# Performance work log

Hardware: AMD Instinct MI355X
Metric: run time of the kernel (lower is better)

Reference implementation:

```python
import jax, jax.numpy as jnp
import numpy as np

B, P, H = 256, 100, 512
NH, HD = 16, 32          # n_head, head_dim
V, N = 20, 200
VN = 1 + V + N           # 221
CSD = 16                 # cur_status_dim
SCALE = HD ** (-0.5)


def setup_inputs() -> dict:
    key = jax.random.key(0)
    ks = jax.random.split(key, 16)
    inp = {
        "q_global": jax.random.normal(ks[0], (B, P, H), jnp.float32),
        "k_global": jax.random.normal(ks[1], (B, NH, VN, HD), jnp.float32),
        "v_global": jax.random.normal(ks[2], (B, NH, VN, HD), jnp.float32),
        "k_node": jax.random.normal(ks[3], (B, NH, 1 + N, HD), jnp.float32),
        "v_node": jax.random.normal(ks[4], (B, NH, 1 + N, HD), jnp.float32),
        "k_vehicle": jax.random.normal(ks[5], (B, NH, 1 + V, HD), jnp.float32),
        "v_vehicle": jax.random.normal(ks[6], (B, NH, 1 + V, HD), jnp.float32),
        "k_vehicle_node": jax.random.normal(ks[7], (B, NH, V, HD), jnp.float32),
        "v_vehicle_node": jax.random.normal(ks[8], (B, NH, V, HD), jnp.float32),
        "context_feature": jax.random.normal(ks[9], (B, P, CSD), jnp.float32),
        "cache_pointer": jax.random.normal(ks[10], (B, H, VN), jnp.float32),
    }
    # random illegal mask; keep the depot column (0) always legal so no row is fully masked
    mask = jax.random.bernoulli(ks[11], 0.3, (B * P, VN))
    inp["illegal_mask"] = mask.at[:, 0].set(False)
    # learned params (torch Linear stores [out, in])
    inp["Wq_w"] = jax.random.normal(ks[12], (H, H + CSD), jnp.float32) * 0.02
    inp["combine_w"] = jax.random.normal(ks[13], (H, H), jnp.float32) * 0.02
    inp["combine_b"] = jax.random.normal(ks[14], (H,), jnp.float32) * 0.02
    return inp


def _attend(q, k, v, mask=None):
    # q: [B,NH,P,HD], k/v: [B,NH,K,HD], mask: [B,P,K] bool (True = illegal)
    scores = jnp.einsum("bhpd,bhkd->bhpk", q, k) * SCALE
    if mask is not None:
        scores = jnp.where(mask[:, None, :, :], -jnp.inf, scores)
    w = jax.nn.softmax(scores, axis=-1)
    ctx = jnp.einsum("bhpk,bhkd->bhpd", w, v)
    return ctx.transpose(0, 2, 1, 3).reshape(q.shape[0], q.shape[2], NH * HD)  # [B,P,H]


def reference(q_global, k_global, v_global, k_node, v_node, k_vehicle, v_vehicle,
              k_vehicle_node, v_vehicle_node, context_feature, cache_pointer,
              illegal_mask, Wq_w, combine_w, combine_b):
    mask = illegal_mask.reshape(B, P, VN)
    q = jnp.concatenate([q_global, context_feature], axis=-1) @ Wq_w.T  # [B,P,H]
    q = q.reshape(B, P, NH, HD).transpose(0, 2, 1, 3)                   # [B,NH,P,HD]
    context = (_attend(q, k_global, v_global, mask)
               + _attend(q, k_node, v_node)
               + _attend(q, k_vehicle, v_vehicle)
               + _attend(q, k_vehicle_node, v_vehicle_node))            # [B,P,H]
    mha_out = context @ combine_w.T + combine_b                          # [B,P,H]
    logits = jnp.einsum("bph,bhk->bpk", mha_out, cache_pointer)          # [B,P,VN]
    return logits.reshape(B * P, VN).astype(jnp.float32)
```

## Files before the change

kernel.cpp:

```cpp
#include <hip/hip_runtime.h>
#include <hip/hip_bf16.h>

#define B_   256
#define P_   100
#define H_   512
#define NH_  16
#define HD_  32
#define VN_  221
#define KNODE 201
#define KVEH  21
#define KVND  20
#define CSD_ 16
#define MASKP 224

typedef __attribute__((ext_vector_type(8))) short short8;
typedef __attribute__((ext_vector_type(4))) float f32x4;

#define K_OFF   0
#define V_OFF   38400
#define ATTN_LDS_B 69632

__device__ __forceinline__ unsigned cvtpk(float lo, float hi) {
    unsigned r;
    asm("v_cvt_pk_bf16_f32 %0, %1, %2" : "=v"(r) : "v"(lo), "v"(hi));
    return r;
}
__device__ __forceinline__ unsigned f2bf(float f) {
    union { float f; unsigned u; } x; x.f = f;
    return (x.u + 0x7FFFu + ((x.u >> 16) & 1u)) >> 16;
}

__global__ void mask_detect_kernel(const unsigned int* __restrict__ w,
                                   int nwords, int* __restrict__ flag) {
    int i = blockIdx.x * 256 + threadIdx.x;
    if (i < nwords && (w[i] & ~1u)) atomicOr(flag, 1);
}

__global__ void mask_repack_kernel(const unsigned char* __restrict__ mb,
                                   const int* __restrict__ mw,
                                   const int* __restrict__ flag,
                                   unsigned char* __restrict__ out) {
    int i = blockIdx.x * blockDim.x + threadIdx.x;
    if (i >= B_ * P_ * MASKP) return;
    int row = i / MASKP, k = i - row * MASKP;
    unsigned char v = 1;
    if (k < VN_) {
        int src = row * VN_ + k;
        v = (*flag) ? (unsigned char)(mb[src] != 0) : (unsigned char)(mw[src] != 0);
    }
    out[i] = v;
}

template<bool MASKED, int C0, int C1, int LO, int HI>
__device__ __forceinline__ void attend_v5(
    const char* __restrict__ ldsb,
    const unsigned* __restrict__ mpre,
    short8 qf, int g, int qr, int addrA, int addrB,
    f32x4& O0, f32x4& O1)
{
    f32x4 A0a = {0.f,0.f,0.f,0.f}, A1a = {0.f,0.f,0.f,0.f};
    f32x4 A0b = {0.f,0.f,0.f,0.f}, A1b = {0.f,0.f,0.f,0.f};
    float ssum = 0.f;
    const bool sel = g < 2;
    #pragma unroll
    for (int c = C0; c <= C1; ++c) {
        const int kb = c * 32;
        short8 kf0 = *(const short8*)(ldsb + K_OFF + (size_t)(kb + qr) * 80 + g * 16);
        short8 kf1 = *(const short8*)(ldsb + K_OFF + (size_t)(kb + 16 + qr) * 80 + g * 16);
        __builtin_amdgcn_s_setprio(1);
        f32x4 s0 = __builtin_amdgcn_mfma_f32_16x16x32_bf16(
                       kf0, qf, (f32x4){0.f,0.f,0.f,0.f}, 0, 0, 0);
        f32x4 s1 = __builtin_amdgcn_mfma_f32_16x16x32_bf16(
                       kf1, qf, (f32x4){0.f,0.f,0.f,0.f}, 0, 0, 0);
        __builtin_amdgcn_s_setprio(0);
        unsigned mdw0 = 0, mdw1 = 0;
        if (MASKED) {
            mdw0 = mpre[2 * (c - C0)];
            mdw1 = mpre[2 * (c - C0) + 1];
        }
        float e0[4], e1[4];
        #pragma unroll
        for (int r = 0; r < 4; ++r) {
            const int key0 = kb + 4 * g + r;
            const int key1 = key0 + 16;
            float x0 = exp2f(s0[r]);
            float x1 = exp2f(s1[r]);
            bool ok0, ok1;
            if (MASKED) {
                ok0 = ((mdw0 >> (8 * r)) & 255u) == 0u;
                ok1 = ((mdw1 >> (8 * r)) & 255u) == 0u;
            } else {
                ok0 = (key0 >= LO) & (key0 < HI);
                ok1 = (key1 >= LO) & (key1 < HI);
            }
            e0[r] = ok0 ? x0 : 0.f;
            e1[r] = ok1 ? x1 : 0.f;
            ssum += e0[r] + e1[r];
        }
        unsigned w0 = cvtpk(e0[0], e0[1]), w1 = cvtpk(e0[2], e0[3]);
        unsigned w2 = cvtpk(e1[0], e1[1]), w3 = cvtpk(e1[2], e1[3]);
        int pA0 = __builtin_amdgcn_ds_bpermute(addrA, (int)w0);
        int pA1 = __builtin_amdgcn_ds_bpermute(addrA, (int)w1);
        int pB0 = __builtin_amdgcn_ds_bpermute(addrB, (int)w0);
        int pB1 = __builtin_amdgcn_ds_bpermute(addrB, (int)w1);
        int qA0 = __builtin_amdgcn_ds_bpermute(addrA, (int)w2);
        int qA1 = __builtin_amdgcn_ds_bpermute(addrA, (int)w3);
        int qB0 = __builtin_amdgcn_ds_bpermute(addrB, (int)w2);
        int qB1 = __builtin_amdgcn_ds_bpermute(addrB, (int)w3);
        union { int u[4]; short8 s8; } pf;
        pf.u[0] = sel ? pA0 : qA0;
        pf.u[1] = sel ? pA1 : qA1;
        pf.u[2] = sel ? pB0 : qB0;
        pf.u[3] = sel ? pB1 : qB1;
        short8 v0 = *(const short8*)(ldsb + V_OFF + (size_t)qr * 976 + kb * 2 + g * 16);
        short8 v1 = *(const short8*)(ldsb + V_OFF + (size_t)(qr + 16) * 976 + kb * 2 + g * 16);
        __builtin_amdgcn_s_setprio(1);
        if (c & 1) {
            A0b = __builtin_amdgcn_mfma_f32_16x16x32_bf16(v0, pf.s8, A0b, 0, 0, 0);
            A1b = __builtin_amdgcn_mfma_f32_16x16x32_bf16(v1, pf.s8, A1b, 0, 0, 0);
        } else {
            A0a = __builtin_amdgcn_mfma_f32_16x16x32_bf16(v0, pf.s8, A0a, 0, 0, 0);
            A1a = __builtin_amdgcn_mfma_f32_16x16x32_bf16(v1, pf.s8, A1a, 0, 0, 0);
        }
        __builtin_amdgcn_s_setprio(0);
    }
    ssum += __shfl_xor(ssum, 16);
    ssum += __shfl_xor(ssum, 32);
    const float inv = 1.f / ssum;
    O0 += (A0a + A0b) * inv;
    O1 += (A1a + A1b) * inv;
}

__global__ __launch_bounds__(512, 4) void attn_mfma_kernel(
    const float* __restrict__ q4,
    const float* __restrict__ kg,  const float* __restrict__ vg,
    const float* __restrict__ kn,  const float* __restrict__ vn,
    const float* __restrict__ kv,  const float* __restrict__ vv,
    const float* __restrict__ kvn, const float* __restrict__ vvn,
    const unsigned char* __restrict__ maskp,
    float* __restrict__ ctx_out)
{
    extern __shared__ char ldsb[];
    const int tid = threadIdx.x;
    const int bh = blockIdx.x, b = bh >> 4, nh = bh & 15;

    const int wave = tid >> 6;
    const int g = (tid >> 4) & 3, qr = tid & 15;
    const int q0 = wave * 16;
    const int qe = (q0 + qr < 100) ? (q0 + qr) : 99;
    const float* qp = q4 + ((size_t)bh * 100 + qe) * 32 + g * 8;
    float4 qa = *(const float4*)qp;
    float4 qc = *(const float4*)(qp + 4);
    const unsigned char* mrow = maskp + ((size_t)b * 100 + qe) * MASKP;
    unsigned mpre[14];
    #pragma unroll
    for (int c = 0; c < 7; ++c) {
        mpre[2 * c]     = *(const unsigned*)(mrow + c * 32 + g * 4);
        mpre[2 * c + 1] = *(const unsigned*)(mrow + c * 32 + 16 + g * 4);
    }

    const float* kg_s  = kg  + (size_t)bh * VN_   * 32;
    const float* kn_s  = kn  + (size_t)bh * KNODE * 32;
    const float* kv_s  = kv  + (size_t)bh * KVEH  * 32;
    const float* kvn_s = kvn + (size_t)bh * KVND  * 32;
    const float* vg_s  = vg  + (size_t)bh * VN_   * 32;
    const float* vn_s  = vn  + (size_t)bh * KNODE * 32;
    const float* vv_s  = vv  + (size_t)bh * KVEH  * 32;
    const float* vvn_s = vvn + (size_t)bh * KVND  * 32;

    {
        float4 ka[4], kc[4];
        int koff[4]; bool kok[4];
        #pragma unroll
        for (int it = 0; it < 4; ++it) {
            int slot = tid + it * 512;
            kok[it] = slot < 1852;
            const float* sp; int li, r0;
            if (slot >= 1772)      { sp = kvn_s; li = slot - 1772; r0 = 456; }
            else if (slot >= 1688) { sp = kv_s;  li = slot - 1688; r0 = 432; }
            else if (slot >= 884)  { sp = kn_s;  li = slot - 884;  r0 = 224; }
            else                   { sp = kg_s;  li = slot;        r0 = 0;   }
            int r = li >> 2, s2 = li & 3;
            koff[it] = (r0 + r) * 80 + s2 * 16;
            if (kok[it]) {
                ka[it] = *(const float4*)(sp + r * 32 + s2 * 8);
                kc[it] = *(const float4*)(sp + r * 32 + s2 * 8 + 4);
            }
        }
        #pragma unroll
        for (int it = 0; it < 4; ++it) {
            if (kok[it]) {
                uint4 w;
                w.x = cvtpk(ka[it].x, ka[it].y); w.y = cvtpk(ka[it].z, ka[it].w);
                w.z = cvtpk(kc[it].x, kc[it].y); w.w = cvtpk(kc[it].z, kc[it].w);
                *(uint4*)(ldsb + K_OFF + koff[it]) = w;
            }
        }
    }
    for (int lin = tid; lin < 17 * 4; lin += 512) {
        int zi = lin >> 2, s = lin & 3;
        int zr = (zi < 3) ? 221 + zi : (zi < 10) ? 422 + zi
               : (zi < 13) ? 443 + zi : 463 + zi;
        *(uint4*)(ldsb + K_OFF + (size_t)zr * 80 + s * 16) = (uint4){0,0,0,0};
    }
    {
        char* vb = ldsb + V_OFF;
        float4 va[4], vb4[4];
        int vd0[4], vk2[4]; bool vok[4];
        #pragma unroll
        for (int it = 0; it < 4; ++it) {
            int slot = tid + it * 512;
            vok[it] = slot < 1840;
            const float* sp; int li, r0;
            if (slot >= 1760)      { sp = vvn_s; li = slot - 1760; r0 = 456; }
            else if (slot >= 1680) { sp = vv_s;  li = slot - 1680; r0 = 432; }
            else if (slot >= 880)  { sp = vn_s;  li = slot - 880;  r0 = 224; }
            else                   { sp = vg_s;  li = slot;        r0 = 0;   }
            int p = li >> 3, dq = li & 7;
            vd0[it] = dq * 4;
            vk2[it] = (r0 + 2 * p) * 2;
            if (vok[it]) {
                va[it]  = *(const float4*)(sp + (2 * p) * 32 + dq * 4);
                vb4[it] = *(const float4*)(sp + (2 * p + 1) * 32 + dq * 4);
            }
        }
        #pragma unroll
        for (int it = 0; it < 4; ++it) {
            if (vok[it]) {
                int d0 = vd0[it], k2 = vk2[it];
                *(unsigned*)(vb + (size_t)(d0 + 0) * 976 + k2) = cvtpk(va[it].x, vb4[it].x);
                *(unsigned*)(vb + (size_t)(d0 + 1) * 976 + k2) = cvtpk(va[it].y, vb4[it].y);
                *(unsigned*)(vb + (size_t)(d0 + 2) * 976 + k2) = cvtpk(va[it].z, vb4[it].z);
                *(unsigned*)(vb + (size_t)(d0 + 3) * 976 + k2) = cvtpk(va[it].w, vb4[it].w);
            }
        }
        if (tid < 32) {
            int d = tid;
            *(unsigned*)(vb + (size_t)d * 976 + 220 * 2) = cvtpk(vg_s[220 * 32 + d], 0.f);
            *(unsigned*)(vb + (size_t)d * 976 + 424 * 2) = cvtpk(vn_s[200 * 32 + d], 0.f);
            *(unsigned*)(vb + (size_t)d * 976 + 452 * 2) = cvtpk(vv_s[20 * 32 + d], 0.f);
        }
        for (int lin = tid; lin < 7 * 32; lin += 512) {
            int pi = lin >> 5, d = lin & 31;
            int pk = (pi == 0) ? 222 : (pi < 4) ? 424 + 2 * pi
                   : (pi == 4) ? 454 : 466 + 2 * pi;
            *(unsigned*)(vb + (size_t)d * 976 + (size_t)pk * 2) = 0;
        }
    }
    __syncthreads();

    if (wave >= 7) return;

    short8 qf;
    {
        const float SC = 0.2550524218f;
        union { unsigned u[4]; short8 s8; } q;
        q.u[0] = cvtpk(qa.x * SC, qa.y * SC);
        q.u[1] = cvtpk(qa.z * SC, qa.w * SC);
        q.u[2] = cvtpk(qc.x * SC, qc.y * SC);
        q.u[3] = cvtpk(qc.z * SC, qc.w * SC);
        qf = q.s8;
    }
    const int addrA = 4 * (qr + ((g & 1) << 5));
    const int addrB = addrA + 64;

    f32x4 O0 = {0.f,0.f,0.f,0.f}, O1 = {0.f,0.f,0.f,0.f};
    attend_v5<true,  0,  6,   0, 224>(ldsb, mpre, qf, g, qr, addrA, addrB, O0, O1);
    attend_v5<false, 7, 13, 224, 425>(ldsb, nullptr, qf, g, qr, addrA, addrB, O0, O1);
    attend_v5<false,13, 14, 432, 453>(ldsb, nullptr, qf, g, qr, addrA, addrB, O0, O1);
    attend_v5<false,14, 14, 456, 476>(ldsb, nullptr, qf, g, qr, addrA, addrB, O0, O1);

    if (q0 + qr < 100) {
        float* op = ctx_out + ((size_t)b * 100 + q0 + qr) * 512 + nh * 32 + 4 * g;
        *(f32x4*)op        = O0;
        *(f32x4*)(op + 16) = O1;
    }
}

template<bool QPROJ>
__global__ __launch_bounds__(512, 4) void gemm_nfused(
    const float* __restrict__ Aq, const float* __restrict__ cf,
    const float* __restrict__ W,  const float* __restrict__ bias,
    float* __restrict__ outp)
{
    __shared__ char As[64 * 80];
    __shared__ char Bs[256 * 80];
    const int tid = threadIdx.x;
    const int n0 = blockIdx.x * 256, m0 = blockIdx.y * 64;
    const int wave = tid >> 6, lane = tid & 63;
    const int wm = wave >> 2, wn = wave & 3;
    const int g = lane >> 4, qr = lane & 15;
    const int ar = tid >> 3, as = tid & 7;
    constexpr int KTOT_ = QPROJ ? 544 : 512;
    constexpr int WSTR  = QPROJ ? 528 : 512;

    f32x4 acc[2][4] = {};
    for (int k0 = 0; k0 < KTOT_; k0 += 32) {
        float4 a4 = {0,0,0,0};
        {
            const int k = k0 + as * 4;
            if (!QPROJ || k < 512) {
                a4 = *(const float4*)(Aq + (size_t)(m0 + ar) * 512 + k);
            } else if (k < 528) {
                a4 = *(const float4*)(cf + (size_t)(m0 + ar) * 16 + (k - 512));
            }
        }
        float4 b0[2], b1[2];
        #pragma unroll
        for (int it = 0; it < 2; ++it) {
            int slot = tid + it * 512;
            int row = slot >> 2, sq = slot & 3;
            int k = k0 + sq * 8;
            b0[it] = (float4){0,0,0,0}; b1[it] = (float4){0,0,0,0};
            if (!QPROJ || k < 528) {
                const float* wp = W + (size_t)(n0 + row) * WSTR + k;
                b0[it] = *(const float4*)wp;
                b1[it] = *(const float4*)(wp + 4);
            }
        }
        __syncthreads();
        {
            uint2 w;
            w.x = cvtpk(a4.x, a4.y); w.y = cvtpk(a4.z, a4.w);
            *(uint2*)(As + ar * 80 + as * 8) = w;
        }
        #pragma unroll
        for (int it = 0; it < 2; ++it) {
            int slot = tid + it * 512;
            int row = slot >> 2, sq = slot & 3;
            uint4 w;
            w.x = cvtpk(b0[it].x, b0[it].y); w.y = cvtpk(b0[it].z, b0[it].w);
            w.z = cvtpk(b1[it].x, b1[it].y); w.w = cvtpk(b1[it].z, b1[it].w);
            *(uint4*)(Bs + row * 80 + sq * 16) = w;
        }
        __syncthreads();
        short8 af0 = *(const short8*)(As + (wm * 32 + qr) * 80 + g * 16);
        short8 af1 = *(const short8*)(As + (wm * 32 + 16 + qr) * 80 + g * 16);
        #pragma unroll
        for (int nj = 0; nj < 4; ++nj) {
            short8 bf = *(const short8*)(Bs + (wn * 64 + nj * 16 + qr) * 80 + g * 16);
            acc[0][nj] = __builtin_amdgcn_mfma_f32_16x16x32_bf16(af0, bf, acc[0][nj], 0, 0, 0);
            acc[1][nj] = __builtin_amdgcn_mfma_f32_16x16x32_bf16(af1, bf, acc[1][nj], 0, 0, 0);
        }
    }
    #pragma unroll
    for (int mi = 0; mi < 2; ++mi)
        #pragma unroll
        for (int nj = 0; nj < 4; ++nj) {
            const int n = n0 + wn * 64 + nj * 16 + qr;
            const float bia = QPROJ ? 0.f : bias[n];
            #pragma unroll
            for (int reg = 0; reg < 4; ++reg) {
                int m = m0 + wm * 32 + 16 * mi + 4 * g + reg;
                if (QPROJ) {
                    int bb = m / 100, p = m - bb * 100;
                    int nh = n >> 5, d = n & 31;
                    outp[(((size_t)bb * NH_ + nh) * P_ + p) * HD_ + d] = acc[mi][nj][reg];
                } else {
                    outp[(size_t)m * 512 + n] = acc[mi][nj][reg] + bia;
                }
            }
        }
}

__global__ __launch_bounds__(512, 4) void logits_mfma(
    const float* __restrict__ mha,
    const float* __restrict__ cp,
    float* __restrict__ out)
{
    __shared__ char As[128 * 80];
    __shared__ char Bs[112 * 80];
    const int b   = blockIdx.x >> 1;
    const int nh0 = (blockIdx.x & 1) * 112;
    const int tid = threadIdx.x;
    const int wave = tid >> 6, lane = tid & 63;
    const int g = lane >> 4, qr = lane & 15;
    const int row = tid >> 2, s = tid & 3;

    f32x4 acc[7] = {};
    for (int h0 = 0; h0 < 512; h0 += 32) {
        float4 a4 = {0,0,0,0}, c4 = {0,0,0,0};
        if (row < 100) {
            const float* mp = mha + ((size_t)b * P_ + row) * 512 + h0 + 8 * s;
            a4 = *(const float4*)mp;
            c4 = *(const float4*)(mp + 4);
        }
        float cv[2][4];
        int ckk[2], chq[2]; bool cok[2];
        #pragma unroll
        for (int it = 0; it < 2; ++it) {
            int slot = tid + it * 512;
            bool in = slot < 896;
            int kkl = in ? (slot % 112) : 0;
            int hq  = in ? (slot / 112) : 0;
            int kk  = nh0 + kkl;
            ckk[it] = kkl; chq[it] = hq;
            cok[it] = in;
            cv[it][0] = cv[it][1] = cv[it][2] = cv[it][3] = 0.f;
            if (in && kk < VN_) {
                const float* cpp = cp + ((size_t)b * 512 + h0 + hq * 4) * VN_ + kk;
                cv[it][0] = cpp[0];
                cv[it][1] = cpp[VN_];
                cv[it][2] = cpp[2 * VN_];
                cv[it][3] = cpp[3 * VN_];
            }
        }
        __syncthreads();
        {
            uint4 w;
            w.x = cvtpk(a4.x, a4.y); w.y = cvtpk(a4.z, a4.w);
            w.z = cvtpk(c4.x, c4.y); w.w = cvtpk(c4.z, c4.w);
            *(uint4*)(As + row * 80 + s * 16) = w;
        }
        #pragma unroll
        for (int it = 0; it < 2; ++it) {
            if (cok[it]) {
                uint2 w;
                w.x = cvtpk(cv[it][0], cv[it][1]);
                w.y = cvtpk(cv[it][2], cv[it][3]);
                *(uint2*)(Bs + ckk[it] * 80 + chq[it] * 8) = w;
            }
        }
        __syncthreads();
        short8 af = *(const short8*)(As + (wave * 16 + qr) * 80 + g * 16);
        #pragma unroll
        for (int ni = 0; ni < 7; ++ni) {
            short8 bf = *(const short8*)(Bs + (ni * 16 + qr) * 80 + g * 16);
            acc[ni] = __builtin_amdgcn_mfma_f32_16x16x32_bf16(af, bf, acc[ni], 0, 0, 0);
        }
    }
    #pragma unroll
    for (int ni = 0; ni < 7; ++ni) {
        int key = nh0 + ni * 16 + qr;
        if (key >= VN_) continue;
        #pragma unroll
        for (int reg = 0; reg < 4; ++reg) {
            int p = wave * 16 + 4 * g + reg;
            if (p < P_)
                out[((size_t)b * P_ + p) * VN_ + key] = acc[ni][reg];
        }
    }
}

extern "C" void kernel_launch(void* const* d_in, const int* in_sizes, int n_in,
                              void* d_out, int out_size, void* d_ws, size_t ws_size,
                              hipStream_t stream) {
    const float* qg   = (const float*)d_in[0];
    const float* kgl  = (const float*)d_in[1];
    const float* vgl  = (const float*)d_in[2];
    const float* knd  = (const float*)d_in[3];
    const float* vnd  = (const float*)d_in[4];
    const float* kvh  = (const float*)d_in[5];
    const float* vvh  = (const float*)d_in[6];
    const float* kvnd = (const float*)d_in[7];
    const float* vvnd = (const float*)d_in[8];
    const float* cf   = (const float*)d_in[9];
    const float* cp   = (const float*)d_in[10];
    const void*  mask_raw = d_in[11];
    const float* Wq   = (const float*)d_in[12];
    const float* Wc   = (const float*)d_in[13];
    const float* bias = (const float*)d_in[14];
    float* out = (float*)d_out;

    const size_t NQ = (size_t)B_ * NH_ * P_ * HD_;
    float* q4buf  = (float*)d_ws;
    float* ctxbuf = q4buf + NQ;
    float* mhabuf = q4buf;
    unsigned char* mask8 = (unsigned char*)(ctxbuf + NQ);
    const int MASKN_P = B_ * P_ * MASKP;
    int* flag = (int*)(mask8 + ((MASKN_P + 15) & ~15));

    hipFuncSetAttribute(reinterpret_cast<const void*>(attn_mfma_kernel),
                        hipFuncAttributeMaxDynamicSharedMemorySize,
                        ATTN_LDS_B);

    hipMemsetAsync(flag, 0, sizeof(int), stream);
    mask_detect_kernel<<<16, 256, 0, stream>>>(
        (const unsigned int*)mask_raw, 4096, flag);
    mask_repack_kernel<<<(MASKN_P + 255) / 256, 256, 0, stream>>>(
        (const unsigned char*)mask_raw, (const int*)mask_raw, flag, mask8);

    gemm_nfused<true><<<dim3(2, 400), 512, 0, stream>>>(qg, cf, Wq, nullptr, q4buf);
    attn_mfma_kernel<<<B_ * NH_, 512, ATTN_LDS_B, stream>>>(
        q4buf, kgl, vgl, knd, vnd, kvh, vvh, kvnd, vvnd, mask8, ctxbuf);
    gemm_nfused<false><<<dim3(2, 400), 512, 0, stream>>>(ctxbuf, nullptr, Wc, bias, mhabuf);
    logits_mfma<<<B_ * 2, 512, 0, stream>>>(mhabuf, cp, out);
}
```

Measured before the change: 337.6 us.

## Make attention kernel persistent with double-buffered LDS prefetch of next head

Replaces the one-block-per-(batch,head) attention launch with 256 persistent blocks, each looping over 16 heads. Each block keeps two LDS buffers and loads the next head's K/V (converted to bf16) and Q while it computes the current one, hiding global load latency behind MFMA work. The mask is now read per chunk instead of prefetched into registers. The cost is twice the LDS per block, which lowers occupancy to one block per CU, and only 256 blocks on a device with more CUs may leave some idle.

New measurement: 691.3 us. 105% more time.

```diff
diff --git a/kernel.cpp b/kernel.cpp
--- a/kernel.cpp
+++ b/kernel.cpp
@@ -19,6 +19,7 @@
 #define K_OFF   0
 #define V_OFF   38400
 #define ATTN_LDS_B 69632
+#define ATTN_LDS_2B (2 * ATTN_LDS_B)
 
 __device__ __forceinline__ unsigned cvtpk(float lo, float hi) {
     unsigned r;
@@ -51,10 +52,108 @@
     out[i] = v;
 }
 
+__device__ __forceinline__ void k_issue(
+    float4 (&ka)[4], float4 (&kc)[4], int (&koff)[4], bool (&kok)[4],
+    int tid, int bh,
+    const float* __restrict__ kg, const float* __restrict__ kn,
+    const float* __restrict__ kv, const float* __restrict__ kvn)
+{
+    const float* kg_s  = kg  + (size_t)bh * VN_   * 32;
+    const float* kn_s  = kn  + (size_t)bh * KNODE * 32;
+    const float* kv_s  = kv  + (size_t)bh * KVEH  * 32;
+    const float* kvn_s = kvn + (size_t)bh * KVND  * 32;
+    #pragma unroll
+    for (int it = 0; it < 4; ++it) {
+        int slot = tid + it * 512;
+        kok[it] = slot < 1852;
+        const float* sp; int li, r0;
+        if (slot >= 1772)      { sp = kvn_s; li = slot - 1772; r0 = 456; }
+        else if (slot >= 1688) { sp = kv_s;  li = slot - 1688; r0 = 432; }
+        else if (slot >= 884)  { sp = kn_s;  li = slot - 884;  r0 = 224; }
+        else                   { sp = kg_s;  li = slot;        r0 = 0;   }
+        int r = li >> 2, s2 = li & 3;
+        koff[it] = (r0 + r) * 80 + s2 * 16;
+        if (kok[it]) {
+            ka[it] = *(const float4*)(sp + r * 32 + s2 * 8);
+            kc[it] = *(const float4*)(sp + r * 32 + s2 * 8 + 4);
+        }
+    }
+}
+__device__ __forceinline__ void k_write(
+    const float4 (&ka)[4], const float4 (&kc)[4],
+    const int (&koff)[4], const bool (&kok)[4], char* __restrict__ ldsb)
+{
+    #pragma unroll
+    for (int it = 0; it < 4; ++it) {
+        if (kok[it]) {
+            uint4 w;
+            w.x = cvtpk(ka[it].x, ka[it].y); w.y = cvtpk(ka[it].z, ka[it].w);
+            w.z = cvtpk(kc[it].x, kc[it].y); w.w = cvtpk(kc[it].z, kc[it].w);
+            *(uint4*)(ldsb + K_OFF + koff[it]) = w;
+        }
+    }
+}
+__device__ __forceinline__ void v_issue(
+    float4 (&va)[4], float4 (&vc)[4], int (&vd0)[4], int (&vk2)[4], bool (&vok)[4],
+    float (&tl)[3],
+    int tid, int bh,
+    const float* __restrict__ vg, const float* __restrict__ vn,
+    const float* __restrict__ vv, const float* __restrict__ vvn)
+{
+    const float* vg_s  = vg  + (size_t)bh * VN_   * 32;
+    const float* vn_s  = vn  + (size_t)bh * KNODE * 32;
+    const float* vv_s  = vv  + (size_t)bh * KVEH  * 32;
+    const float* vvn_s = vvn + (size_t)bh * KVND  * 32;
+    #pragma unroll
+    for (int it = 0; it < 4; ++it) {
+        int slot = tid + it * 512;
+        vok[it] = slot < 1840;
+        const float* sp; int li, r0;
+        if (slot >= 1760)      { sp = vvn_s; li = slot - 1760; r0 = 456; }
+        else if (slot >= 1680) { sp = vv_s;  li = slot - 1680; r0 = 432; }
+        else if (slot >= 880)  { sp = vn_s;  li = slot - 880;  r0 = 224; }
+        else                   { sp = vg_s;  li = slot;        r0 = 0;   }
+        int p = li >> 3, dq = li & 7;
+        vd0[it] = dq * 4;
+        vk2[it] = (r0 + 2 * p) * 2;
+        if (vok[it]) {
+            va[it] = *(const float4*)(sp + (2 * p) * 32 + dq * 4);
+            vc[it] = *(const float4*)(sp + (2 * p + 1) * 32 + dq * 4);
+        }
+    }
+    if (tid < 32) {
+        tl[0] = vg_s[220 * 32 + tid];
+        tl[1] = vn_s[200 * 32 + tid];
+        tl[2] = vv_s[20 * 32 + tid];
+    }
+}
+__device__ __forceinline__ void v_write(
+    const float4 (&va)[4], const float4 (&vc)[4],
+    const int (&vd0)[4], const int (&vk2)[4], const bool (&vok)[4],
+    const float (&tl)[3], char* __restrict__ ldsb, int tid)
+{
+    char* vb = ldsb + V_OFF;
+    #pragma unroll
+    for (int it = 0; it < 4; ++it) {
+        if (vok[it]) {
+            int d0 = vd0[it], k2 = vk2[it];
+            *(unsigned*)(vb + (size_t)(d0 + 0) * 976 + k2) = cvtpk(va[it].x, vc[it].x);
+            *(unsigned*)(vb + (size_t)(d0 + 1) * 976 + k2) = cvtpk(va[it].y, vc[it].y);
+            *(unsigned*)(vb + (size_t)(d0 + 2) * 976 + k2) = cvtpk(va[it].z, vc[it].z);
+            *(unsigned*)(vb + (size_t)(d0 + 3) * 976 + k2) = cvtpk(va[it].w, vc[it].w);
+        }
+    }
+    if (tid < 32) {
+        *(unsigned*)(vb + (size_t)tid * 976 + 220 * 2) = cvtpk(tl[0], 0.f);
+        *(unsigned*)(vb + (size_t)tid * 976 + 424 * 2) = cvtpk(tl[1], 0.f);
+        *(unsigned*)(vb + (size_t)tid * 976 + 452 * 2) = cvtpk(tl[2], 0.f);
+    }
+}
+
 template<bool MASKED, int C0, int C1, int LO, int HI>
-__device__ __forceinline__ void attend_v5(
+__device__ __forceinline__ void attend_v6(
     const char* __restrict__ ldsb,
-    const unsigned* __restrict__ mpre,
+    const unsigned char* __restrict__ mrow,
     short8 qf, int g, int qr, int addrA, int addrB,
     f32x4& O0, f32x4& O1)
 {
@@ -75,8 +174,8 @@
         __builtin_amdgcn_s_setprio(0);
         unsigned mdw0 = 0, mdw1 = 0;
         if (MASKED) {
-            mdw0 = mpre[2 * (c - C0)];
-            mdw1 = mpre[2 * (c - C0) + 1];
+            mdw0 = *(const unsigned*)(mrow + kb + g * 4);
+            mdw1 = *(const unsigned*)(mrow + kb + 16 + g * 4);
         }
         float e0[4], e1[4];
         #pragma unroll
@@ -131,7 +230,7 @@
     O1 += (A1a + A1b) * inv;
 }
 
-__global__ __launch_bounds__(512, 4) void attn_mfma_kernel(
+__global__ __launch_bounds__(512, 4) void attn_persist(
     const float* __restrict__ q4,
     const float* __restrict__ kg,  const float* __restrict__ vg,
     const float* __restrict__ kn,  const float* __restrict__ vn,
@@ -140,106 +239,24 @@
     const unsigned char* __restrict__ maskp,
     float* __restrict__ ctx_out)
 {
-    extern __shared__ char ldsb[];
+    extern __shared__ char lds2[];
     const int tid = threadIdx.x;
-    const int bh = blockIdx.x, b = bh >> 4, nh = bh & 15;
-
-    const int wave = tid >> 6;
-    const int g = (tid >> 4) & 3, qr = tid & 15;
+    const int wave = tid >> 6, g = (tid >> 4) & 3, qr = tid & 15;
     const int q0 = wave * 16;
     const int qe = (q0 + qr < 100) ? (q0 + qr) : 99;
-    const float* qp = q4 + ((size_t)bh * 100 + qe) * 32 + g * 8;
-    float4 qa = *(const float4*)qp;
-    float4 qc = *(const float4*)(qp + 4);
-    const unsigned char* mrow = maskp + ((size_t)b * 100 + qe) * MASKP;
-    unsigned mpre[14];
-    #pragma unroll
-    for (int c = 0; c < 7; ++c) {
-        mpre[2 * c]     = *(const unsigned*)(mrow + c * 32 + g * 4);
-        mpre[2 * c + 1] = *(const unsigned*)(mrow + c * 32 + 16 + g * 4);
-    }
-
-    const float* kg_s  = kg  + (size_t)bh * VN_   * 32;
-    const float* kn_s  = kn  + (size_t)bh * KNODE * 32;
-    const float* kv_s  = kv  + (size_t)bh * KVEH  * 32;
-    const float* kvn_s = kvn + (size_t)bh * KVND  * 32;
-    const float* vg_s  = vg  + (size_t)bh * VN_   * 32;
-    const float* vn_s  = vn  + (size_t)bh * KNODE * 32;
-    const float* vv_s  = vv  + (size_t)bh * KVEH  * 32;
-    const float* vvn_s = vvn + (size_t)bh * KVND  * 32;
-
-    {
-        float4 ka[4], kc[4];
-        int koff[4]; bool kok[4];
-        #pragma unroll
-        for (int it = 0; it < 4; ++it) {
-            int slot = tid + it * 512;
-            kok[it] = slot < 1852;
-            const float* sp; int li, r0;
-            if (slot >= 1772)      { sp = kvn_s; li = slot - 1772; r0 = 456; }
-            else if (slot >= 1688) { sp = kv_s;  li = slot - 1688; r0 = 432; }
-            else if (slot >= 884)  { sp = kn_s;  li = slot - 884;  r0 = 224; }
-            else                   { sp = kg_s;  li = slot;        r0 = 0;   }
-            int r = li >> 2, s2 = li & 3;
-            koff[it] = (r0 + r) * 80 + s2 * 16;
-            if (kok[it]) {
-                ka[it] = *(const float4*)(sp + r * 32 + s2 * 8);
-                kc[it] = *(const float4*)(sp + r * 32 + s2 * 8 + 4);
-            }
-        }
-        #pragma unroll
-        for (int it = 0; it < 4; ++it) {
-            if (kok[it]) {
-                uint4 w;
-                w.x = cvtpk(ka[it].x, ka[it].y); w.y = cvtpk(ka[it].z, ka[it].w);
-                w.z = cvtpk(kc[it].x, kc[it].y); w.w = cvtpk(kc[it].z, kc[it].w);
-                *(uint4*)(ldsb + K_OFF + koff[it]) = w;
-            }
-        }
-    }
-    for (int lin = tid; lin < 17 * 4; lin += 512) {
-        int zi = lin >> 2, s = lin & 3;
-        int zr = (zi < 3) ? 221 + zi : (zi < 10) ? 422 + zi
-               : (zi < 13) ? 443 + zi : 463 + zi;
-        *(uint4*)(ldsb + K_OFF + (size_t)zr * 80 + s * 16) = (uint4){0,0,0,0};
-    }
-    {
+    const int addrA = 4 * (qr + ((g & 1) << 5));
+    const int addrB = addrA + 64;
+
+    #pragma unroll
+    for (int bi = 0; bi < 2; ++bi) {
+        char* ldsb = lds2 + bi * ATTN_LDS_B;
+        for (int lin = tid; lin < 17 * 4; lin += 512) {
+            int zi = lin >> 2, s = lin & 3;
+            int zr = (zi < 3) ? 221 + zi : (zi < 10) ? 422 + zi
+                   : (zi < 13) ? 443 + zi : 463 + zi;
+            *(uint4*)(ldsb + K_OFF + (size_t)zr * 80 + s * 16) = (uint4){0,0,0,0};
+        }
         char* vb = ldsb + V_OFF;
-        float4 va[4], vb4[4];
-        int vd0[4], vk2[4]; bool vok[4];
-        #pragma unroll
-        for (int it = 0; it < 4; ++it) {
-            int slot = tid + it * 512;
-            vok[it] = slot < 1840;
-            const float* sp; int li, r0;
-            if (slot >= 1760)      { sp = vvn_s; li = slot - 1760; r0 = 456; }
-            else if (slot >= 1680) { sp = vv_s;  li = slot - 1680; r0 = 432; }
-            else if (slot >= 880)  { sp = vn_s;  li = slot - 880;  r0 = 224; }
-            else                   { sp = vg_s;  li = slot;        r0 = 0;   }
-            int p = li >> 3, dq = li & 7;
-            vd0[it] = dq * 4;
-            vk2[it] = (r0 + 2 * p) * 2;
-            if (vok[it]) {
-                va[it]  = *(const float4*)(sp + (2 * p) * 32 + dq * 4);
-                vb4[it] = *(const float4*)(sp + (2 * p + 1) * 32 + dq * 4);
-            }
-        }
-        #pragma unroll
-        for (int it = 0; it < 4; ++it) {
-            if (vok[it]) {
-                int d0 = vd0[it], k2 = vk2[it];
-                *(unsigned*)(vb + (size_t)(d0 + 0) * 976 + k2) = cvtpk(va[it].x, vb4[it].x);
-                *(unsigned*)(vb + (size_t)(d0 + 1) * 976 + k2) = cvtpk(va[it].y, vb4[it].y);
-                *(unsigned*)(vb + (size_t)(d0 + 2) * 976 + k2) = cvtpk(va[it].z, vb4[it].z);
-                *(unsigned*)(vb + (size_t)(d0 + 3) * 976 + k2) = cvtpk(va[it].w, vb4[it].w);
-            }
-        }
-        if (tid < 32) {
-            int d = tid;
-            *(unsigned*)(vb + (size_t)d * 976 + 220 * 2) = cvtpk(vg_s[220 * 32 + d], 0.f);
-            *(unsigned*)(vb + (size_t)d * 976 + 424 * 2) = cvtpk(vn_s[200 * 32 + d], 0.f);
-            *(unsigned*)(vb + (size_t)d * 976 + 452 * 2) = cvtpk(vv_s[20 * 32 + d], 0.f);
-        }
         for (int lin = tid; lin < 7 * 32; lin += 512) {
             int pi = lin >> 5, d = lin & 31;
             int pk = (pi == 0) ? 222 : (pi < 4) ? 424 + 2 * pi
@@ -247,33 +264,66 @@
             *(unsigned*)(vb + (size_t)d * 976 + (size_t)pk * 2) = 0;
         }
     }
+
+    float4 ka[4], kc[4]; int koff[4]; bool kok[4];
+    float4 va[4], vc[4]; int vd0[4], vk2[4]; bool vok[4]; float tl[3];
+
+    const int t0i = blockIdx.x;
+    k_issue(ka, kc, koff, kok, tid, t0i, kg, kn, kv, kvn);
+    v_issue(va, vc, vd0, vk2, vok, tl, tid, t0i, vg, vn, vv, vvn);
+    float4 qa = *(const float4*)(q4 + ((size_t)t0i * 100 + qe) * 32 + g * 8);
+    float4 qc = *(const float4*)(q4 + ((size_t)t0i * 100 + qe) * 32 + g * 8 + 4);
+    k_write(ka, kc, koff, kok, lds2);
+    v_write(va, vc, vd0, vk2, vok, tl, lds2, tid);
     __syncthreads();
 
-    if (wave >= 7) return;
-
-    short8 qf;
-    {
-        const float SC = 0.2550524218f;
-        union { unsigned u[4]; short8 s8; } q;
-        q.u[0] = cvtpk(qa.x * SC, qa.y * SC);
-        q.u[1] = cvtpk(qa.z * SC, qa.w * SC);
-        q.u[2] = cvtpk(qc.x * SC, qc.y * SC);
-        q.u[3] = cvtpk(qc.z * SC, qc.w * SC);
-        qf = q.s8;
-    }
-    const int addrA = 4 * (qr + ((g & 1) << 5));
-    const int addrB = addrA + 64;
-
-    f32x4 O0 = {0.f,0.f,0.f,0.f}, O1 = {0.f,0.f,0.f,0.f};
-    attend_v5<true,  0,  6,   0, 224>(ldsb, mpre, qf, g, qr, addrA, addrB, O0, O1);
-    attend_v5<false, 7, 13, 224, 425>(ldsb, nullptr, qf, g, qr, addrA, addrB, O0, O1);
-    attend_v5<false,13, 14, 432, 453>(ldsb, nullptr, qf, g, qr, addrA, addrB, O0, O1);
-    attend_v5<false,14, 14, 456, 476>(ldsb, nullptr, qf, g, qr, addrA, addrB, O0, O1);
-
-    if (q0 + qr < 100) {
-        float* op = ctx_out + ((size_t)b * 100 + q0 + qr) * 512 + nh * 32 + 4 * g;
-        *(f32x4*)op        = O0;
-        *(f32x4*)(op + 16) = O1;
+    int cur = 0;
+    for (int t = t0i; t < B_ * NH_; t += 256) {
+        const int tn = t + 256;
+        const bool nxt = tn < B_ * NH_;
+        char* ldsc = lds2 + cur * ATTN_LDS_B;
+        char* ldsa = lds2 + (cur ^ 1) * ATTN_LDS_B;
+        const int b = t >> 4, nh = t & 15;
+        const unsigned char* mrow = maskp + ((size_t)b * 100 + qe) * MASKP;
+
+        short8 qf;
+        {
+            const float SC = 0.2550524218f;
+            union { unsigned u[4]; short8 s8; } q;
+            q.u[0] = cvtpk(qa.x * SC, qa.y * SC);
+            q.u[1] = cvtpk(qa.z * SC, qa.w * SC);
+            q.u[2] = cvtpk(qc.x * SC, qc.y * SC);
+            q.u[3] = cvtpk(qc.z * SC, qc.w * SC);
+            qf = q.s8;
+        }
+
+        float4 qa_n = {0,0,0,0}, qc_n = {0,0,0,0};
+        if (nxt) {
+            k_issue(ka, kc, koff, kok, tid, tn, kg, kn, kv, kvn);
+            const float* qp = q4 + ((size_t)tn * 100 + qe) * 32 + g * 8;
+            qa_n = *(const float4*)qp;
+            qc_n = *(const float4*)(qp + 4);
+        }
+        f32x4 O0 = {0.f,0.f,0.f,0.f}, O1 = {0.f,0.f,0.f,0.f};
+        if (wave < 7)
+            attend_v6<true, 0, 6, 0, 224>(ldsc, mrow, qf, g, qr, addrA, addrB, O0, O1);
+        if (nxt) k_write(ka, kc, koff, kok, ldsa);
+
+        if (nxt) v_issue(va, vc, vd0, vk2, vok, tl, tid, tn, vg, vn, vv, vvn);
+        if (wave < 7) {
+            attend_v6<false, 7, 13, 224, 425>(ldsc, mrow, qf, g, qr, addrA, addrB, O0, O1);
+            attend_v6<false,13, 14, 432, 453>(ldsc, mrow, qf, g, qr, addrA, addrB, O0, O1);
+            attend_v6<false,14, 14, 456, 476>(ldsc, mrow, qf, g, qr, addrA, addrB, O0, O1);
+            if (q0 + qr < 100) {
+                float* op = ctx_out + ((size_t)b * 100 + q0 + qr) * 512 + nh * 32 + 4 * g;
+                *(f32x4*)op        = O0;
+                *(f32x4*)(op + 16) = O1;
+            }
+        }
+        if (nxt) v_write(va, vc, vd0, vk2, vok, tl, ldsa, tid);
+        __syncthreads();
+        cur ^= 1;
+        qa = qa_n; qc = qc_n;
     }
 }
 
@@ -470,9 +520,9 @@
     const int MASKN_P = B_ * P_ * MASKP;
     int* flag = (int*)(mask8 + ((MASKN_P + 15) & ~15));
 
-    hipFuncSetAttribute(reinterpret_cast<const void*>(attn_mfma_kernel),
+    hipFuncSetAttribute(reinterpret_cast<const void*>(attn_persist),
                         hipFuncAttributeMaxDynamicSharedMemorySize,
-                        ATTN_LDS_B);
+                        ATTN_LDS_2B);
 
     hipMemsetAsync(flag, 0, sizeof(int), stream);
     mask_detect_kernel<<<16, 256, 0, stream>>>(
@@ -481,7 +531,7 @@
         (const unsigned char*)mask_raw, (const int*)mask_raw, flag, mask8);
 
     gemm_nfused<true><<<dim3(2, 400), 512, 0, stream>>>(qg, cf, Wq, nullptr, q4buf);
-    attn_mfma_kernel<<<B_ * NH_, 512, ATTN_LDS_B, stream>>>(
+    attn_persist<<<256, 512, ATTN_LDS_2B, stream>>>(
         q4buf, kgl, vgl, knd, vnd, kvh, vvh, kvnd, vvnd, mask8, ctxbuf);
     gemm_nfused<false><<<dim3(2, 400), 512, 0, stream>>>(ctxbuf, nullptr, Wc, bias, mhabuf);
     logits_mfma<<<B_ * 2, 512, 0, stream>>>(mhabuf, cp, out);
```

## Split attention kernel into global-masked and rest kernels with smaller LDS

Applied to the files above, without the earlier changes.

The single attention kernel that staged all four K/V sets into about 68 KB of LDS is split into two kernels. One handles the node/vehicle/vehicle-node attentions and writes ctx. The other handles the masked global attention and does a read-add-write into ctx. Each kernel uses roughly 33-38 KB of static LDS with launch bounds raised to 8 blocks per CU, aiming for more resident blocks and better latency hiding. The cost is an extra launch, reloading q and the full ctx write/read round trip through global memory.

New measurement: 507.5 us. 1.5x slower.

```diff
diff --git a/kernel.cpp b/kernel.cpp
--- a/kernel.cpp
+++ b/kernel.cpp
@@ -16,9 +16,12 @@
 typedef __attribute__((ext_vector_type(8))) short short8;
 typedef __attribute__((ext_vector_type(4))) float f32x4;
 
-#define K_OFF   0
-#define V_OFF   38400
-#define ATTN_LDS_B 69632
+#define H0_VOFF 17920
+#define H0_VSTR 464
+#define H0_LDS  (H0_VOFF + 32 * H0_VSTR)
+#define H1_VOFF 20480
+#define H1_VSTR 528
+#define H1_LDS  (H1_VOFF + 32 * H1_VSTR)
 
 __device__ __forceinline__ unsigned cvtpk(float lo, float hi) {
     unsigned r;
@@ -51,7 +54,7 @@
     out[i] = v;
 }
 
-template<bool MASKED, int C0, int C1, int LO, int HI>
+template<bool MASKED, int C0, int C1, int LO, int HI, int VOFF, int VSTR>
 __device__ __forceinline__ void attend_v5(
     const char* __restrict__ ldsb,
     const unsigned* __restrict__ mpre,
@@ -65,8 +68,8 @@
     #pragma unroll
     for (int c = C0; c <= C1; ++c) {
         const int kb = c * 32;
-        short8 kf0 = *(const short8*)(ldsb + K_OFF + (size_t)(kb + qr) * 80 + g * 16);
-        short8 kf1 = *(const short8*)(ldsb + K_OFF + (size_t)(kb + 16 + qr) * 80 + g * 16);
+        short8 kf0 = *(const short8*)(ldsb + (size_t)(kb + qr) * 80 + g * 16);
+        short8 kf1 = *(const short8*)(ldsb + (size_t)(kb + 16 + qr) * 80 + g * 16);
         __builtin_amdgcn_s_setprio(1);
         f32x4 s0 = __builtin_amdgcn_mfma_f32_16x16x32_bf16(
                        kf0, qf, (f32x4){0.f,0.f,0.f,0.f}, 0, 0, 0);
@@ -112,8 +115,8 @@
         pf.u[1] = sel ? pA1 : qA1;
         pf.u[2] = sel ? pB0 : qB0;
         pf.u[3] = sel ? pB1 : qB1;
-        short8 v0 = *(const short8*)(ldsb + V_OFF + (size_t)qr * 976 + kb * 2 + g * 16);
-        short8 v1 = *(const short8*)(ldsb + V_OFF + (size_t)(qr + 16) * 976 + kb * 2 + g * 16);
+        short8 v0 = *(const short8*)(ldsb + VOFF + (size_t)qr * VSTR + kb * 2 + g * 16);
+        short8 v1 = *(const short8*)(ldsb + VOFF + (size_t)(qr + 16) * VSTR + kb * 2 + g * 16);
         __builtin_amdgcn_s_setprio(1);
         if (c & 1) {
             A0b = __builtin_amdgcn_mfma_f32_16x16x32_bf16(v0, pf.s8, A0b, 0, 0, 0);
@@ -131,21 +134,142 @@
     O1 += (A1a + A1b) * inv;
 }
 
-__global__ __launch_bounds__(512, 4) void attn_mfma_kernel(
+__global__ __launch_bounds__(512, 8) void attn_rest(
     const float* __restrict__ q4,
-    const float* __restrict__ kg,  const float* __restrict__ vg,
     const float* __restrict__ kn,  const float* __restrict__ vn,
     const float* __restrict__ kv,  const float* __restrict__ vv,
     const float* __restrict__ kvn, const float* __restrict__ vvn,
+    float* __restrict__ ctx_out)
+{
+    __shared__ char ldsb[H1_LDS];
+    const int tid = threadIdx.x;
+    const int bh = blockIdx.x, b = bh >> 4, nh = bh & 15;
+    const int wave = tid >> 6, g = (tid >> 4) & 3, qr = tid & 15;
+    const int q0 = wave * 16;
+    const int qe = (q0 + qr < 100) ? (q0 + qr) : 99;
+    const float* qp = q4 + ((size_t)bh * 100 + qe) * 32 + g * 8;
+    float4 qa = *(const float4*)qp;
+    float4 qc = *(const float4*)(qp + 4);
+
+    const float* kn_s  = kn  + (size_t)bh * KNODE * 32;
+    const float* kv_s  = kv  + (size_t)bh * KVEH  * 32;
+    const float* kvn_s = kvn + (size_t)bh * KVND  * 32;
+    const float* vn_s  = vn  + (size_t)bh * KNODE * 32;
+    const float* vv_s  = vv  + (size_t)bh * KVEH  * 32;
+    const float* vvn_s = vvn + (size_t)bh * KVND  * 32;
+
+    {
+        float4 ka[2], kc[2]; int koff[2]; bool kok[2];
+        #pragma unroll
+        for (int it = 0; it < 2; ++it) {
+            int slot = tid + it * 512;
+            kok[it] = slot < 968;
+            const float* sp; int li, r0;
+            if (slot >= 888)      { sp = kvn_s; li = slot - 888; r0 = 232; }
+            else if (slot >= 804) { sp = kv_s;  li = slot - 804; r0 = 208; }
+            else                  { sp = kn_s;  li = slot;       r0 = 0;   }
+            int r = li >> 2, s2 = li & 3;
+            koff[it] = (r0 + r) * 80 + s2 * 16;
+            if (kok[it]) {
+                ka[it] = *(const float4*)(sp + r * 32 + s2 * 8);
+                kc[it] = *(const float4*)(sp + r * 32 + s2 * 8 + 4);
+            }
+        }
+        #pragma unroll
+        for (int it = 0; it < 2; ++it) {
+            if (kok[it]) {
+                uint4 w;
+                w.x = cvtpk(ka[it].x, ka[it].y); w.y = cvtpk(ka[it].z, ka[it].w);
+                w.z = cvtpk(kc[it].x, kc[it].y); w.w = cvtpk(kc[it].z, kc[it].w);
+                *(uint4*)(ldsb + koff[it]) = w;
+            }
+        }
+    }
+    if (tid < 56) {
+        int zi = tid >> 2, s = tid & 3;
+        int zr = (zi < 7) ? 201 + zi : (zi < 10) ? 222 + zi : 242 + zi;
+        *(uint4*)(ldsb + (size_t)zr * 80 + s * 16) = (uint4){0,0,0,0};
+    }
+    {
+        char* vb = ldsb + H1_VOFF;
+        float4 va[2], vc[2]; int vd0[2], vk2[2]; bool vok[2];
+        #pragma unroll
+        for (int it = 0; it < 2; ++it) {
+            int slot = tid + it * 512;
+            vok[it] = slot < 960;
+            const float* sp; int li, r0;
+            if (slot >= 880)      { sp = vvn_s; li = slot - 880; r0 = 232; }
+            else if (slot >= 800) { sp = vv_s;  li = slot - 800; r0 = 208; }
+            else                  { sp = vn_s;  li = slot;       r0 = 0;   }
+            int p = li >> 3, dq = li & 7;
+            vd0[it] = dq * 4;
+            vk2[it] = (r0 + 2 * p) * 2;
+            if (vok[it]) {
+                va[it] = *(const float4*)(sp + (2 * p) * 32 + dq * 4);
+                vc[it] = *(const float4*)(sp + (2 * p + 1) * 32 + dq * 4);
+            }
+        }
+        #pragma unroll
+        for (int it = 0; it < 2; ++it) {
+            if (vok[it]) {
+                int d0 = vd0[it], k2 = vk2[it];
+                *(unsigned*)(vb + (size_t)(d0 + 0) * H1_VSTR + k2) = cvtpk(va[it].x, vc[it].x);
+                *(unsigned*)(vb + (size_t)(d0 + 1) * H1_VSTR + k2) = cvtpk(va[it].y, vc[it].y);
+                *(unsigned*)(vb + (size_t)(d0 + 2) * H1_VSTR + k2) = cvtpk(va[it].z, vc[it].z);
+                *(unsigned*)(vb + (size_t)(d0 + 3) * H1_VSTR + k2) = cvtpk(va[it].w, vc[it].w);
+            }
+        }
+        if (tid < 32) {
+            int d = tid;
+            *(unsigned*)(vb + (size_t)d * H1_VSTR + 400) = cvtpk(vn_s[200 * 32 + d], 0.f);
+            *(unsigned*)(vb + (size_t)d * H1_VSTR + 456) = cvtpk(vv_s[20 * 32 + d], 0.f);
+        }
+        if (tid < 192) {
+            int pi = tid >> 5, d = tid & 31;
+            int pk = (pi == 0) ? 202 : (pi == 1) ? 204 : (pi == 2) ? 206
+                   : (pi == 3) ? 230 : (pi == 4) ? 252 : 254;
+            *(unsigned*)(vb + (size_t)d * H1_VSTR + (size_t)pk * 2) = 0;
+        }
+    }
+    __syncthreads();
+
+    if (wave >= 7) return;
+
+    short8 qf;
+    {
+        const float SC = 0.2550524218f;
+        union { unsigned u[4]; short8 s8; } q;
+        q.u[0] = cvtpk(qa.x * SC, qa.y * SC);
+        q.u[1] = cvtpk(qa.z * SC, qa.w * SC);
+        q.u[2] = cvtpk(qc.x * SC, qc.y * SC);
+        q.u[3] = cvtpk(qc.z * SC, qc.w * SC);
+        qf = q.s8;
+    }
+    const int addrA = 4 * (qr + ((g & 1) << 5));
+    const int addrB = addrA + 64;
+
+    f32x4 O0 = {0.f,0.f,0.f,0.f}, O1 = {0.f,0.f,0.f,0.f};
+    attend_v5<false, 0, 6,   0, 201, H1_VOFF, H1_VSTR>(ldsb, nullptr, qf, g, qr, addrA, addrB, O0, O1);
+    attend_v5<false, 6, 7, 208, 229, H1_VOFF, H1_VSTR>(ldsb, nullptr, qf, g, qr, addrA, addrB, O0, O1);
+    attend_v5<false, 7, 7, 232, 252, H1_VOFF, H1_VSTR>(ldsb, nullptr, qf, g, qr, addrA, addrB, O0, O1);
+
+    if (q0 + qr < 100) {
+        float* op = ctx_out + ((size_t)b * 100 + q0 + qr) * 512 + nh * 32 + 4 * g;
+        *(f32x4*)op        = O0;
+        *(f32x4*)(op + 16) = O1;
+    }
+}
+
+__global__ __launch_bounds__(512, 8) void attn_global(
+    const float* __restrict__ q4,
+    const float* __restrict__ kg, const float* __restrict__ vg,
     const unsigned char* __restrict__ maskp,
     float* __restrict__ ctx_out)
 {
-    extern __shared__ char ldsb[];
+    __shared__ char ldsb[H0_LDS];
     const int tid = threadIdx.x;
     const int bh = blockIdx.x, b = bh >> 4, nh = bh & 15;
-
-    const int wave = tid >> 6;
-    const int g = (tid >> 4) & 3, qr = tid & 15;
+    const int wave = tid >> 6, g = (tid >> 4) & 3, qr = tid & 15;
     const int q0 = wave * 16;
     const int qe = (q0 + qr < 100) ? (q0 + qr) : 99;
     const float* qp = q4 + ((size_t)bh * 100 + qe) * 32 + g * 8;
@@ -159,92 +283,65 @@
         mpre[2 * c + 1] = *(const unsigned*)(mrow + c * 32 + 16 + g * 4);
     }
 
-    const float* kg_s  = kg  + (size_t)bh * VN_   * 32;
-    const float* kn_s  = kn  + (size_t)bh * KNODE * 32;
-    const float* kv_s  = kv  + (size_t)bh * KVEH  * 32;
-    const float* kvn_s = kvn + (size_t)bh * KVND  * 32;
-    const float* vg_s  = vg  + (size_t)bh * VN_   * 32;
-    const float* vn_s  = vn  + (size_t)bh * KNODE * 32;
-    const float* vv_s  = vv  + (size_t)bh * KVEH  * 32;
-    const float* vvn_s = vvn + (size_t)bh * KVND  * 32;
+    const float* kg_s = kg + (size_t)bh * VN_ * 32;
+    const float* vg_s = vg + (size_t)bh * VN_ * 32;
 
     {
-        float4 ka[4], kc[4];
-        int koff[4]; bool kok[4];
-        #pragma unroll
-        for (int it = 0; it < 4; ++it) {
-            int slot = tid + it * 512;
-            kok[it] = slot < 1852;
-            const float* sp; int li, r0;
-            if (slot >= 1772)      { sp = kvn_s; li = slot - 1772; r0 = 456; }
-            else if (slot >= 1688) { sp = kv_s;  li = slot - 1688; r0 = 432; }
-            else if (slot >= 884)  { sp = kn_s;  li = slot - 884;  r0 = 224; }
-            else                   { sp = kg_s;  li = slot;        r0 = 0;   }
-            int r = li >> 2, s2 = li & 3;
-            koff[it] = (r0 + r) * 80 + s2 * 16;
+        float4 ka[2], kc[2]; int koff[2]; bool kok[2];
+        #pragma unroll
+        for (int it = 0; it < 2; ++it) {
+            int slot = tid + it * 512;
+            kok[it] = slot < 884;
+            int r = slot >> 2, s2 = slot & 3;
+            koff[it] = r * 80 + s2 * 16;
             if (kok[it]) {
-                ka[it] = *(const float4*)(sp + r * 32 + s2 * 8);
-                kc[it] = *(const float4*)(sp + r * 32 + s2 * 8 + 4);
-            }
-        }
-        #pragma unroll
-        for (int it = 0; it < 4; ++it) {
+                ka[it] = *(const float4*)(kg_s + r * 32 + s2 * 8);
+                kc[it] = *(const float4*)(kg_s + r * 32 + s2 * 8 + 4);
+            }
+        }
+        #pragma unroll
+        for (int it = 0; it < 2; ++it) {
             if (kok[it]) {
                 uint4 w;
                 w.x = cvtpk(ka[it].x, ka[it].y); w.y = cvtpk(ka[it].z, ka[it].w);
                 w.z = cvtpk(kc[it].x, kc[it].y); w.w = cvtpk(kc[it].z, kc[it].w);
-                *(uint4*)(ldsb + K_OFF + koff[it]) = w;
-            }
-        }
-    }
-    for (int lin = tid; lin < 17 * 4; lin += 512) {
-        int zi = lin >> 2, s = lin & 3;
-        int zr = (zi < 3) ? 221 + zi : (zi < 10) ? 422 + zi
-               : (zi < 13) ? 443 + zi : 463 + zi;
-        *(uint4*)(ldsb + K_OFF + (size_t)zr * 80 + s * 16) = (uint4){0,0,0,0};
+                *(uint4*)(ldsb + koff[it]) = w;
+            }
+        }
+    }
+    if (tid < 12) {
+        int zi = tid >> 2, s = tid & 3;
+        *(uint4*)(ldsb + (size_t)(221 + zi) * 80 + s * 16) = (uint4){0,0,0,0};
     }
     {
-        char* vb = ldsb + V_OFF;
-        float4 va[4], vb4[4];
-        int vd0[4], vk2[4]; bool vok[4];
-        #pragma unroll
-        for (int it = 0; it < 4; ++it) {
-            int slot = tid + it * 512;
-            vok[it] = slot < 1840;
-            const float* sp; int li, r0;
-            if (slot >= 1760)      { sp = vvn_s; li = slot - 1760; r0 = 456; }
-            else if (slot >= 1680) { sp = vv_s;  li = slot - 1680; r0 = 432; }
-            else if (slot >= 880)  { sp = vn_s;  li = slot - 880;  r0 = 224; }
-            else                   { sp = vg_s;  li = slot;        r0 = 0;   }
-            int p = li >> 3, dq = li & 7;
+        char* vb = ldsb + H0_VOFF;
+        float4 va[2], vc[2]; int vd0[2], vk2[2]; bool vok[2];
+        #pragma unroll
+        for (int it = 0; it < 2; ++it) {
+            int slot = tid + it * 512;
+            vok[it] = slot < 880;
+            int p = slot >> 3, dq = slot & 7;
             vd0[it] = dq * 4;
-            vk2[it] = (r0 + 2 * p) * 2;
+            vk2[it] = (2 * p) * 2;
             if (vok[it]) {
-                va[it]  = *(const float4*)(sp + (2 * p) * 32 + dq * 4);
-                vb4[it] = *(const float4*)(sp + (2 * p + 1) * 32 + dq * 4);
-            }
-        }
-        #pragma unroll
-        for (int it = 0; it < 4; ++it) {
+                va[it] = *(const float4*)(vg_s + (2 * p) * 32 + dq * 4);
+                vc[it] = *(const float4*)(vg_s + (2 * p + 1) * 32 + dq * 4);
+            }
+        }
+        #pragma unroll
+        for (int it = 0; it < 2; ++it) {
             if (vok[it]) {
                 int d0 = vd0[it], k2 = vk2[it];
-                *(unsigned*)(vb + (size_t)(d0 + 0) * 976 + k2) = cvtpk(va[it].x, vb4[it].x);
-                *(unsigned*)(vb + (size_t)(d0 + 1) * 976 + k2) = cvtpk(va[it].y, vb4[it].y);
-                *(unsigned*)(vb + (size_t)(d0 + 2) * 976 + k2) = cvtpk(va[it].z, vb4[it].z);
-                *(unsigned*)(vb + (size_t)(d0 + 3) * 976 + k2) = cvtpk(va[it].w, vb4[it].w);
+                *(unsigned*)(vb + (size_t)(d0 + 0) * H0_VSTR + k2) = cvtpk(va[it].x, vc[it].x);
+                *(unsigned*)(vb + (size_t)(d0 + 1) * H0_VSTR + k2) = cvtpk(va[it].y, vc[it].y);
+                *(unsigned*)(vb + (size_t)(d0 + 2) * H0_VSTR + k2) = cvtpk(va[it].z, vc[it].z);
+                *(unsigned*)(vb + (size_t)(d0 + 3) * H0_VSTR + k2) = cvtpk(va[it].w, vc[it].w);
             }
         }
         if (tid < 32) {
             int d = tid;
-            *(unsigned*)(vb + (size_t)d * 976 + 220 * 2) = cvtpk(vg_s[220 * 32 + d], 0.f);
-            *(unsigned*)(vb + (size_t)d * 976 + 424 * 2) = cvtpk(vn_s[200 * 32 + d], 0.f);
-            *(unsigned*)(vb + (size_t)d * 976 + 452 * 2) = cvtpk(vv_s[20 * 32 + d], 0.f);
-        }
-        for (int lin = tid; lin < 7 * 32; lin += 512) {
-            int pi = lin >> 5, d = lin & 31;
-            int pk = (pi == 0) ? 222 : (pi < 4) ? 424 + 2 * pi
-                   : (pi == 4) ? 454 : 466 + 2 * pi;
-            *(unsigned*)(vb + (size_t)d * 976 + (size_t)pk * 2) = 0;
+            *(unsigned*)(vb + (size_t)d * H0_VSTR + 440) = cvtpk(vg_s[220 * 32 + d], 0.f);
+            *(unsigned*)(vb + (size_t)d * H0_VSTR + 444) = 0;
         }
     }
     __syncthreads();
@@ -265,15 +362,14 @@
     const int addrB = addrA + 64;
 
     f32x4 O0 = {0.f,0.f,0.f,0.f}, O1 = {0.f,0.f,0.f,0.f};
-    attend_v5<true,  0,  6,   0, 224>(ldsb, mpre, qf, g, qr, addrA, addrB, O0, O1);
-    attend_v5<false, 7, 13, 224, 425>(ldsb, nullptr, qf, g, qr, addrA, addrB, O0, O1);
-    attend_v5<false,13, 14, 432, 453>(ldsb, nullptr, qf, g, qr, addrA, addrB, O0, O1);
-    attend_v5<false,14, 14, 456, 476>(ldsb, nullptr, qf, g, qr, addrA, addrB, O0, O1);
+    attend_v5<true, 0, 6, 0, 224, H0_VOFF, H0_VSTR>(ldsb, mpre, qf, g, qr, addrA, addrB, O0, O1);
 
     if (q0 + qr < 100) {
         float* op = ctx_out + ((size_t)b * 100 + q0 + qr) * 512 + nh * 32 + 4 * g;
-        *(f32x4*)op        = O0;
-        *(f32x4*)(op + 16) = O1;
+        f32x4 p0 = *(const f32x4*)op;
+        f32x4 p1 = *(const f32x4*)(op + 16);
+        *(f32x4*)op        = p0 + O0;
+        *(f32x4*)(op + 16) = p1 + O1;
     }
 }
 
@@ -470,10 +566,6 @@
     const int MASKN_P = B_ * P_ * MASKP;
     int* flag = (int*)(mask8 + ((MASKN_P + 15) & ~15));
 
-    hipFuncSetAttribute(reinterpret_cast<const void*>(attn_mfma_kernel),
-                        hipFuncAttributeMaxDynamicSharedMemorySize,
-                        ATTN_LDS_B);
-
     hipMemsetAsync(flag, 0, sizeof(int), stream);
     mask_detect_kernel<<<16, 256, 0, stream>>>(
         (const unsigned int*)mask_raw, 4096, flag);
@@ -481,8 +573,10 @@
         (const unsigned char*)mask_raw, (const int*)mask_raw, flag, mask8);
 
     gemm_nfused<true><<<dim3(2, 400), 512, 0, stream>>>(qg, cf, Wq, nullptr, q4buf);
-    attn_mfma_kernel<<<B_ * NH_, 512, ATTN_LDS_B, stream>>>(
-        q4buf, kgl, vgl, knd, vnd, kvh, vvh, kvnd, vvnd, mask8, ctxbuf);
+    attn_rest<<<B_ * NH_, 512, 0, stream>>>(
+        q4buf, knd, vnd, kvh, vvh, kvnd, vvnd, ctxbuf);
+    attn_global<<<B_ * NH_, 512, 0, stream>>>(
+        q4buf, kgl, vgl, mask8, ctxbuf);
     gemm_nfused<false><<<dim3(2, 400), 512, 0, stream>>>(ctxbuf, nullptr, Wc, bias, mhabuf);
     logits_mfma<<<B_ * 2, 512, 0, stream>>>(mhabuf, cp, out);
 }
```
